# Kernel tuning notes

Measured on AMD Instinct MI355X. Metric: run time of the kernel, lower is better.

## Reference

```python
import jax, jax.numpy as jnp
import numpy as np

N_A, N_B, N_C = 100000, 60000, 40000
N = N_A + N_B + N_C  # 200000 total nodes after concat
E = 3200000
D_IN = (512, 256, 128)
D = 64  # com_feat_dim == emb_dim


def setup_inputs() -> dict:
    key = jax.random.key(0)
    ks = jax.random.split(key, 16)
    inp = {
        "feat_a": jax.random.normal(ks[0], (N_A, D_IN[0]), jnp.float32),
        "W_a": jax.random.normal(ks[1], (D_IN[0], D), jnp.float32) * 0.05,
        "b_a": jax.random.normal(ks[2], (D,), jnp.float32) * 0.05,
        "feat_b": jax.random.normal(ks[3], (N_B, D_IN[1]), jnp.float32),
        "W_b": jax.random.normal(ks[4], (D_IN[1], D), jnp.float32) * 0.05,
        "b_b": jax.random.normal(ks[5], (D,), jnp.float32) * 0.05,
        "feat_c": jax.random.normal(ks[6], (N_C, D_IN[2]), jnp.float32),
        "W_c": jax.random.normal(ks[7], (D_IN[2], D), jnp.float32) * 0.05,
        "b_c": jax.random.normal(ks[8], (D,), jnp.float32) * 0.05,
        "gcn_W": jax.random.normal(ks[9], (D, D), jnp.float32) * 0.1,
        "gcn_b": jax.random.normal(ks[10], (D,), jnp.float32) * 0.05,
        "edge_weight": jax.random.uniform(ks[11], (E,), jnp.float32),
        "edge_src": jax.random.randint(ks[12], (E,), 0, N, jnp.int32),
        "edge_dst": jax.random.randint(ks[13], (E,), 0, N, jnp.int32),
    }
    return inp


def reference(feat_a, W_a, b_a, feat_b, W_b, b_b, feat_c, W_c, b_c,
              gcn_W, gcn_b, edge_weight, edge_src, edge_dst):
    # Per-type linear encoders + ReLU, then concat over the node axis
    enc = jnp.concatenate([
        jax.nn.relu(feat_a @ W_a + b_a),
        jax.nn.relu(feat_b @ W_b + b_b),
        jax.nn.relu(feat_c @ W_c + b_c),
    ], axis=0)  # [N, D]
    # GraphConvolution: out = spmm(adj, enc @ W + b)
    support = enc @ gcn_W + gcn_b                    # [N, D]
    msg = support[edge_src] * edge_weight[:, None]   # [E, D] irregular gather
    com_emb = jax.ops.segment_sum(msg, edge_dst, num_segments=N)  # [N, D]
    # F.normalize(p=2, dim=1)
    norm = jnp.linalg.norm(com_emb, axis=1, keepdims=True)
    com_emb = com_emb / jnp.maximum(norm, 1e-12)
    return com_emb
```

## Files before the change

### kernel.cpp

```cpp
#include <hip/hip_runtime.h>

#define N_A 100000
#define N_B 60000
#define N_C 40000
#define NTOT 200000
#define NEDGE 3200000
#define D 64

#define SCAN_BLK 1024
#define NB_SCAN ((NTOT + SCAN_BLK - 1) / SCAN_BLK)

template <int K, bool RELU>
__global__ __launch_bounds__(256) void gemm64_kernel(
    const float* __restrict__ X, const float* __restrict__ W,
    const float* __restrict__ bias, float* __restrict__ Y,
    int Nn, int node0out)
{
    __shared__ float sF[32][260];
    __shared__ float sW[32 * 64];

    const int tid = threadIdx.x;
    const int td  = tid & 7;
    const int tn  = tid >> 3;
    const int d0  = td * 8;
    const int n0  = tn * 8;
    const int blockNode = blockIdx.x * 256;

    float acc[8][8] = {};

    for (int k0 = 0; k0 < K; k0 += 32) {
        {
            const float4* gw = (const float4*)(W + (long long)k0 * 64);
#pragma unroll
            for (int i = 0; i < 2; ++i) {
                const int idx = i * 256 + tid;
                ((float4*)sW)[idx] = gw[idx];
            }
        }
        {
            const int tk = tid & 7;
            const int nl = tid >> 3;
#pragma unroll
            for (int p = 0; p < 8; ++p) {
                const int n  = p * 32 + nl;
                const int gn = blockNode + n;
                float4 f = make_float4(0.f, 0.f, 0.f, 0.f);
                if (gn < Nn)
                    f = *(const float4*)(X + (long long)gn * K + k0 + tk * 4);
                sF[tk * 4 + 0][n] = f.x;
                sF[tk * 4 + 1][n] = f.y;
                sF[tk * 4 + 2][n] = f.z;
                sF[tk * 4 + 3][n] = f.w;
            }
        }
        __syncthreads();

#pragma unroll 4
        for (int kk = 0; kk < 32; ++kk) {
            const float4 w0 = *(const float4*)(sW + kk * 64 + d0);
            const float4 w1 = *(const float4*)(sW + kk * 64 + d0 + 4);
            const float4 f0 = *(const float4*)(&sF[kk][n0]);
            const float4 f1 = *(const float4*)(&sF[kk][n0 + 4]);
            float wv[8] = { w0.x, w0.y, w0.z, w0.w, w1.x, w1.y, w1.z, w1.w };
            float fv[8] = { f0.x, f0.y, f0.z, f0.w, f1.x, f1.y, f1.z, f1.w };
#pragma unroll
            for (int j = 0; j < 8; ++j)
#pragma unroll
                for (int i = 0; i < 8; ++i)
                    acc[j][i] = fmaf(fv[j], wv[i], acc[j][i]);
        }
        __syncthreads();
    }

    float bv[8];
    *(float4*)&bv[0] = *(const float4*)(bias + d0);
    *(float4*)&bv[4] = *(const float4*)(bias + d0 + 4);
#pragma unroll
    for (int j = 0; j < 8; ++j) {
        const int gn = blockNode + n0 + j;
        if (gn < Nn) {
            float o[8];
#pragma unroll
            for (int i = 0; i < 8; ++i) {
                o[i] = acc[j][i] + bv[i];
                if (RELU) o[i] = fmaxf(o[i], 0.f);
            }
            float* yp = Y + (long long)(node0out + gn) * 64 + d0;
            *(float4*)(yp)     = *(float4*)&o[0];
            *(float4*)(yp + 4) = *(float4*)&o[4];
        }
    }
}

__global__ void zero_ints(int* __restrict__ p, int n)
{
    int i = blockIdx.x * blockDim.x + threadIdx.x;
    if (i < n) p[i] = 0;
}

__global__ void hist_kernel(const int* __restrict__ edst, int* __restrict__ deg, int e)
{
    int i  = blockIdx.x * blockDim.x + threadIdx.x;
    int st = gridDim.x * blockDim.x;
    for (; i < e; i += st) atomicAdd(&deg[edst[i]], 1);
}

__global__ __launch_bounds__(SCAN_BLK) void s1_blocksums(const int* __restrict__ deg,
                                                         int* __restrict__ partials, int n)
{
    const int tid = threadIdx.x;
    const int i   = blockIdx.x * SCAN_BLK + tid;
    int v = (i < n) ? deg[i] : 0;
#pragma unroll
    for (int o = 32; o; o >>= 1) v += __shfl_xor(v, o, 64);
    __shared__ int wsum[SCAN_BLK / 64];
    if ((tid & 63) == 0) wsum[tid >> 6] = v;
    __syncthreads();
    if (tid == 0) {
        int s = 0;
#pragma unroll
        for (int w = 0; w < SCAN_BLK / 64; ++w) s += wsum[w];
        partials[blockIdx.x] = s;
    }
}

__global__ __launch_bounds__(256) void s2_scan(const int* __restrict__ partials,
                                               int* __restrict__ pscan, int np)
{
    __shared__ int arr[512];
    if (threadIdx.x < np) arr[threadIdx.x] = partials[threadIdx.x];
    __syncthreads();
    if (threadIdx.x == 0) {
        int run = 0;
        for (int i = 0; i < np; ++i) { int t = arr[i]; arr[i] = run; run += t; }
    }
    __syncthreads();
    if (threadIdx.x < np) pscan[threadIdx.x] = arr[threadIdx.x];
}

__global__ __launch_bounds__(SCAN_BLK) void s3_scan(const int* __restrict__ deg,
                                                    const int* __restrict__ pscan,
                                                    int* __restrict__ row_start,
                                                    int* __restrict__ cursor, int n)
{
    const int tid  = threadIdx.x;
    const int lane = tid & 63, wid = tid >> 6;
    const int i    = blockIdx.x * SCAN_BLK + tid;
    int v = (i < n) ? deg[i] : 0;
    int x = v;
#pragma unroll
    for (int o = 1; o < 64; o <<= 1) {
        int y = __shfl_up(x, o, 64);
        if (lane >= o) x += y;
    }
    __shared__ int wsum[SCAN_BLK / 64];
    if (lane == 63) wsum[wid] = x;
    __syncthreads();
    if (tid == 0) {
        int run = 0;
#pragma unroll
        for (int w = 0; w < SCAN_BLK / 64; ++w) { int t = wsum[w]; wsum[w] = run; run += t; }
    }
    __syncthreads();
    if (i < n) {
        const int excl = x - v + wsum[wid] + pscan[blockIdx.x];
        row_start[i] = excl;
        cursor[i]    = excl;
    }
}

__global__ void fill_kernel(const int* __restrict__ esrc, const int* __restrict__ edst,
                            const float* __restrict__ ew, int* __restrict__ cursor,
                            uint2* __restrict__ csr, int e)
{
    int i  = blockIdx.x * blockDim.x + threadIdx.x;
    int st = gridDim.x * blockDim.x;
    for (; i < e; i += st) {
        const int t   = edst[i];
        const int pos = atomicAdd(&cursor[t], 1);
        csr[pos] = make_uint2((unsigned)esrc[i], __float_as_uint(ew[i]));
    }
}

__global__ __launch_bounds__(256) void gather_norm_kernel(const float* __restrict__ support,
                                                          const uint2* __restrict__ csr,
                                                          const int* __restrict__ row_start,
                                                          const int* __restrict__ deg,
                                                          float* __restrict__ out)
{
    const int lane = threadIdx.x & 63;
    const int nid  = blockIdx.x * 4 + (threadIdx.x >> 6);
    if (nid >= NTOT) return;
    const int base = row_start[nid];
    const int dg   = deg[nid];

    float acc = 0.f;
    int i = 0;
    for (; i + 4 <= dg; i += 4) {
        const uint2 c0 = csr[base + i + 0];
        const uint2 c1 = csr[base + i + 1];
        const uint2 c2 = csr[base + i + 2];
        const uint2 c3 = csr[base + i + 3];
        const float v0 = support[(long long)c0.x * D + lane];
        const float v1 = support[(long long)c1.x * D + lane];
        const float v2 = support[(long long)c2.x * D + lane];
        const float v3 = support[(long long)c3.x * D + lane];
        acc = fmaf(v0, __uint_as_float(c0.y), acc);
        acc = fmaf(v1, __uint_as_float(c1.y), acc);
        acc = fmaf(v2, __uint_as_float(c2.y), acc);
        acc = fmaf(v3, __uint_as_float(c3.y), acc);
    }
    for (; i < dg; ++i) {
        const uint2 c = csr[base + i];
        acc = fmaf(support[(long long)c.x * D + lane], __uint_as_float(c.y), acc);
    }

    float ss = acc * acc;
#pragma unroll
    for (int o = 32; o; o >>= 1) ss += __shfl_xor(ss, o, 64);
    const float nrm = fmaxf(sqrtf(ss), 1e-12f);
    out[(long long)nid * D + lane] = acc / nrm;
}

__global__ void zero_kernel(float4* __restrict__ p, long long n4)
{
    long long i  = (long long)blockIdx.x * blockDim.x + threadIdx.x;
    long long st = (long long)gridDim.x * blockDim.x;
    for (; i < n4; i += st) p[i] = float4{0.f, 0.f, 0.f, 0.f};
}

__global__ void scatter_kernel(const float* __restrict__ support,
                               const float* __restrict__ ew,
                               const int* __restrict__ esrc,
                               const int* __restrict__ edst,
                               float* __restrict__ out, int E)
{
    const int d  = threadIdx.x & 63;
    int gw       = blockIdx.x * (blockDim.x >> 6) + (threadIdx.x >> 6);
    const int nw = gridDim.x * (blockDim.x >> 6);
    for (int e = gw; e < E; e += nw) {
        const int   s  = esrc[e];
        const int   t  = edst[e];
        const float we = ew[e];
        atomicAdd(&out[(long long)t * 64 + d], support[(long long)s * 64 + d] * we);
    }
}

__global__ void normalize_kernel(float* __restrict__ out, int N)
{
    const int d   = threadIdx.x & 63;
    const int row = blockIdx.x * (blockDim.x >> 6) + (threadIdx.x >> 6);
    if (row < N) {
        const long long base = (long long)row * 64;
        float x  = out[base + d];
        float ss = x * x;
#pragma unroll
        for (int o = 32; o; o >>= 1) ss += __shfl_xor(ss, o, 64);
        const float nrm = fmaxf(sqrtf(ss), 1e-12f);
        out[base + d] = x / nrm;
    }
}

extern "C" void kernel_launch(void* const* d_in, const int* in_sizes, int n_in,
                              void* d_out, int out_size, void* d_ws, size_t ws_size,
                              hipStream_t stream)
{
    const float* feat_a = (const float*)d_in[0];
    const float* W_a    = (const float*)d_in[1];
    const float* b_a    = (const float*)d_in[2];
    const float* feat_b = (const float*)d_in[3];
    const float* W_b    = (const float*)d_in[4];
    const float* b_b    = (const float*)d_in[5];
    const float* feat_c = (const float*)d_in[6];
    const float* W_c    = (const float*)d_in[7];
    const float* b_c    = (const float*)d_in[8];
    const float* gcn_W  = (const float*)d_in[9];
    const float* gcn_b  = (const float*)d_in[10];
    const float* ew     = (const float*)d_in[11];
    const int*   esrc   = (const int*)d_in[12];
    const int*   edst   = (const int*)d_in[13];

    float* out = (float*)d_out;

    char* ws = (char*)d_ws;
    const size_t off_support = 0;
    const size_t off_deg     = off_support + (size_t)NTOT * D * 4;
    const size_t off_rowst   = off_deg   + (size_t)NTOT * 4;
    const size_t off_cursor  = off_rowst + (size_t)NTOT * 4;
    const size_t off_part    = off_cursor + (size_t)NTOT * 4;
    const size_t off_pscan   = off_part  + 1024;
    const size_t off_csr     = off_pscan + 1024;
    const size_t need        = off_csr + (size_t)NEDGE * 8;

    float* support = (float*)(ws + off_support);

    gemm64_kernel<512, true ><<<(N_A  + 255) / 256, 256, 0, stream>>>(feat_a, W_a, b_a, out, N_A, 0);
    gemm64_kernel<256, true ><<<(N_B  + 255) / 256, 256, 0, stream>>>(feat_b, W_b, b_b, out, N_B, N_A);
    gemm64_kernel<128, true ><<<(N_C  + 255) / 256, 256, 0, stream>>>(feat_c, W_c, b_c, out, N_C, N_A + N_B);
    gemm64_kernel< 64, false><<<(NTOT + 255) / 256, 256, 0, stream>>>(out, gcn_W, gcn_b, support, NTOT, 0);

    if (ws_size >= need) {
        int*   deg     = (int*)(ws + off_deg);
        int*   rowst   = (int*)(ws + off_rowst);
        int*   cursor  = (int*)(ws + off_cursor);
        int*   part    = (int*)(ws + off_part);
        int*   pscan   = (int*)(ws + off_pscan);
        uint2* csr     = (uint2*)(ws + off_csr);

        zero_ints<<<(NTOT + 255) / 256, 256, 0, stream>>>(deg, NTOT);
        hist_kernel<<<4096, 256, 0, stream>>>(edst, deg, NEDGE);
        s1_blocksums<<<NB_SCAN, SCAN_BLK, 0, stream>>>(deg, part, NTOT);
        s2_scan<<<1, 256, 0, stream>>>(part, pscan, NB_SCAN);
        s3_scan<<<NB_SCAN, SCAN_BLK, 0, stream>>>(deg, pscan, rowst, cursor, NTOT);
        fill_kernel<<<4096, 256, 0, stream>>>(esrc, edst, ew, cursor, csr, NEDGE);

        gather_norm_kernel<<<(NTOT + 3) / 4, 256, 0, stream>>>(support, csr, rowst, deg, out);
    } else {
        zero_kernel<<<2048, 256, 0, stream>>>((float4*)out, (long long)NTOT * D / 4);
        scatter_kernel<<<8192, 256, 0, stream>>>(support, ew, esrc, edst, out, NEDGE);
        normalize_kernel<<<NTOT / 4, 256, 0, stream>>>(out, NTOT);
    }
}
```

Before: 1.112 ms.

## Register-prefetch next K tile in encoder GEMMs and shrink blocks to 128 nodes

The encoder and GCN GEMM kernels now load the next 32-wide K slice of features and weights into registers while the current slice is being computed, so global loads overlap the FMA loop. Blocks drop from 256 to 128 threads and 128 nodes each. The feature tile is stored row-major with padding (128x33) rather than transposed, which lets threads write it contiguously. The cost is scalar LDS reads in the inner loop, extra register pressure from the prefetch buffers, and a smaller per-block tile that may reduce weight reuse.

After: 1.056 ms. -5.1%, faster.

```diff
diff --git a/kernel.cpp b/kernel.cpp
--- a/kernel.cpp
+++ b/kernel.cpp
@@ -11,73 +11,84 @@
 #define NB_SCAN ((NTOT + SCAN_BLK - 1) / SCAN_BLK)
 
 template <int K, bool RELU>
-__global__ __launch_bounds__(256) void gemm64_kernel(
+__global__ __launch_bounds__(128) void gemm128_kernel(
     const float* __restrict__ X, const float* __restrict__ W,
     const float* __restrict__ bias, float* __restrict__ Y,
     int Nn, int node0out)
 {
-    __shared__ float sF[32][260];
+    __shared__ float sF[128][33];
     __shared__ float sW[32 * 64];
 
-    const int tid = threadIdx.x;
-    const int td  = tid & 7;
-    const int tn  = tid >> 3;
-    const int d0  = td * 8;
-    const int n0  = tn * 8;
-    const int blockNode = blockIdx.x * 256;
-
-    float acc[8][8] = {};
+    const int tid  = threadIdx.x;
+    const int rql  = tid & 7;
+    const int rowi = tid >> 3;
+    const int tn   = tid >> 3;
+    const int td   = tid & 7;
+    const int n0   = tn * 8;
+    const int d0   = td * 8;
+    const int bn   = blockIdx.x * 128;
+
+    float  acc[8][8] = {};
+    float4 pf[8];
+    float4 pw[4];
+
+#define LOAD_F(k0_)                                                          \
+    _Pragma("unroll")                                                        \
+    for (int p = 0; p < 8; ++p) {                                            \
+        const int gn = bn + rowi + 16 * p;                                   \
+        pf[p] = (gn < Nn)                                                    \
+            ? *(const float4*)(X + (long long)gn * K + (k0_) + rql * 4)      \
+            : make_float4(0.f, 0.f, 0.f, 0.f);                               \
+    }
+#define LOAD_W(k0_)                                                          \
+    {                                                                        \
+        const float4* gw = (const float4*)(W + (long long)(k0_) * 64);       \
+        _Pragma("unroll")                                                    \
+        for (int c = 0; c < 4; ++c) pw[c] = gw[c * 128 + tid];               \
+    }
+
+    LOAD_F(0)
+    LOAD_W(0)
 
     for (int k0 = 0; k0 < K; k0 += 32) {
-        {
-            const float4* gw = (const float4*)(W + (long long)k0 * 64);
-#pragma unroll
-            for (int i = 0; i < 2; ++i) {
-                const int idx = i * 256 + tid;
-                ((float4*)sW)[idx] = gw[idx];
-            }
+        __syncthreads();
+#pragma unroll
+        for (int p = 0; p < 8; ++p) {
+            const int r = rowi + 16 * p;
+            sF[r][rql * 4 + 0] = pf[p].x;
+            sF[r][rql * 4 + 1] = pf[p].y;
+            sF[r][rql * 4 + 2] = pf[p].z;
+            sF[r][rql * 4 + 3] = pf[p].w;
         }
-        {
-            const int tk = tid & 7;
-            const int nl = tid >> 3;
-#pragma unroll
-            for (int p = 0; p < 8; ++p) {
-                const int n  = p * 32 + nl;
-                const int gn = blockNode + n;
-                float4 f = make_float4(0.f, 0.f, 0.f, 0.f);
-                if (gn < Nn)
-                    f = *(const float4*)(X + (long long)gn * K + k0 + tk * 4);
-                sF[tk * 4 + 0][n] = f.x;
-                sF[tk * 4 + 1][n] = f.y;
-                sF[tk * 4 + 2][n] = f.z;
-                sF[tk * 4 + 3][n] = f.w;
-            }
-        }
+#pragma unroll
+        for (int c = 0; c < 4; ++c) ((float4*)sW)[c * 128 + tid] = pw[c];
         __syncthreads();
+        if (k0 + 32 < K) { LOAD_F(k0 + 32) LOAD_W(k0 + 32) }
 
 #pragma unroll 4
         for (int kk = 0; kk < 32; ++kk) {
             const float4 w0 = *(const float4*)(sW + kk * 64 + d0);
             const float4 w1 = *(const float4*)(sW + kk * 64 + d0 + 4);
-            const float4 f0 = *(const float4*)(&sF[kk][n0]);
-            const float4 f1 = *(const float4*)(&sF[kk][n0 + 4]);
-            float wv[8] = { w0.x, w0.y, w0.z, w0.w, w1.x, w1.y, w1.z, w1.w };
-            float fv[8] = { f0.x, f0.y, f0.z, f0.w, f1.x, f1.y, f1.z, f1.w };
+            const float wv[8] = { w0.x, w0.y, w0.z, w0.w, w1.x, w1.y, w1.z, w1.w };
+            float fv[8];
+#pragma unroll
+            for (int j = 0; j < 8; ++j) fv[j] = sF[n0 + j][kk];
 #pragma unroll
             for (int j = 0; j < 8; ++j)
 #pragma unroll
                 for (int i = 0; i < 8; ++i)
                     acc[j][i] = fmaf(fv[j], wv[i], acc[j][i]);
         }
-        __syncthreads();
-    }
+    }
+#undef LOAD_F
+#undef LOAD_W
 
     float bv[8];
     *(float4*)&bv[0] = *(const float4*)(bias + d0);
     *(float4*)&bv[4] = *(const float4*)(bias + d0 + 4);
 #pragma unroll
     for (int j = 0; j < 8; ++j) {
-        const int gn = blockNode + n0 + j;
+        const int gn = bn + n0 + j;
         if (gn < Nn) {
             float o[8];
 #pragma unroll
@@ -239,10 +250,8 @@
     int gw       = blockIdx.x * (blockDim.x >> 6) + (threadIdx.x >> 6);
     const int nw = gridDim.x * (blockDim.x >> 6);
     for (int e = gw; e < E; e += nw) {
-        const int   s  = esrc[e];
-        const int   t  = edst[e];
-        const float we = ew[e];
-        atomicAdd(&out[(long long)t * 64 + d], support[(long long)s * 64 + d] * we);
+        atomicAdd(&out[(long long)edst[e] * 64 + d],
+                  support[(long long)esrc[e] * 64 + d] * ew[e]);
     }
 }
 
@@ -256,8 +265,7 @@
         float ss = x * x;
 #pragma unroll
         for (int o = 32; o; o >>= 1) ss += __shfl_xor(ss, o, 64);
-        const float nrm = fmaxf(sqrtf(ss), 1e-12f);
-        out[base + d] = x / nrm;
+        out[base + d] = x / fmaxf(sqrtf(ss), 1e-12f);
     }
 }
 
@@ -294,10 +302,10 @@
 
     float* support = (float*)(ws + off_support);
 
-    gemm64_kernel<512, true ><<<(N_A  + 255) / 256, 256, 0, stream>>>(feat_a, W_a, b_a, out, N_A, 0);
-    gemm64_kernel<256, true ><<<(N_B  + 255) / 256, 256, 0, stream>>>(feat_b, W_b, b_b, out, N_B, N_A);
-    gemm64_kernel<128, true ><<<(N_C  + 255) / 256, 256, 0, stream>>>(feat_c, W_c, b_c, out, N_C, N_A + N_B);
-    gemm64_kernel< 64, false><<<(NTOT + 255) / 256, 256, 0, stream>>>(out, gcn_W, gcn_b, support, NTOT, 0);
+    gemm128_kernel<512, true ><<<(N_A  + 127) / 128, 128, 0, stream>>>(feat_a, W_a, b_a, out, N_A, 0);
+    gemm128_kernel<256, true ><<<(N_B  + 127) / 128, 128, 0, stream>>>(feat_b, W_b, b_b, out, N_B, N_A);
+    gemm128_kernel<128, true ><<<(N_C  + 127) / 128, 128, 0, stream>>>(feat_c, W_c, b_c, out, N_C, N_A + N_B);
+    gemm128_kernel< 64, false><<<(NTOT + 127) / 128, 128, 0, stream>>>(out, gcn_W, gcn_b, support, NTOT, 0);
 
     if (ws_size >= need) {
         int*   deg     = (int*)(ws + off_deg);
```
